# Kernel tuning notes

Measured on AMD Instinct MI355X. Metric: run time of the kernel, lower is better.

The kernel has to match this reference:

```python
import jax, jax.numpy as jnp
import numpy as np

N, C, H, W = 32, 512, 32, 32
S = 2048
INFLUENCE = 1.0  # influence_decay='constant', training_progress irrelevant


def setup_inputs() -> dict:
    key = jax.random.key(0)
    k1, k2 = jax.random.split(key)
    x = jax.random.normal(k1, (N, C, H, W), dtype=jnp.float32)
    # nn.Parameter(torch.randn(S, C) / C)
    codebook = jax.random.normal(k2, (S, C), dtype=jnp.float32) / C
    return {"x": x, "codebook": codebook}


def _distances(x_flat, codebook):
    # x_flat: [N, C, P], codebook: [S, C] -> [N, S, P]
    # same math as ((x[:,None]-cb[None,...,None])**2).sum(2), without the
    # [N, S, C, P] intermediate
    x2 = jnp.sum(x_flat * x_flat, axis=1)          # [N, P]
    c2 = jnp.sum(codebook * codebook, axis=1)      # [S]
    xc = jnp.einsum('ncp,sc->nsp', x_flat, codebook)  # [N, S, P]
    return x2[:, None, :] + c2[None, :, None] - 2.0 * xc


def reference(x, codebook):
    n, c = x.shape[:2]
    x_flat = x.reshape(n, c, -1)                      # [N, C, P]
    xs = jax.lax.stop_gradient(x_flat)                # distance(x_flat.detach())
    d = _distances(xs, codebook)                      # [N, S, P]
    idx = jnp.argmin(d, axis=1)                       # [N, P]
    xq = jnp.transpose(codebook[idx], (0, 2, 1)).reshape(x.shape)  # [N,C,H,W]
    loss_commitment = jnp.mean((x - jax.lax.stop_gradient(xq)) ** 2)
    d_sorted = jnp.sort(d, axis=1)                    # ascending over S
    w = jnp.exp(-jnp.arange(d.shape[1], dtype=jnp.float32) / INFLUENCE)
    loss_codebook = jnp.mean(w[None, :, None] * d_sorted)
    codebook_indices = idx.reshape(n, *x.shape[2:])   # [N, H, W]
    output = x + jax.lax.stop_gradient(xq - x)        # straight-through
    return (loss_codebook, loss_commitment, codebook_indices, output)
```

## Files before the change

kernel.cpp:

```cpp
#include <hip/hip_runtime.h>
#include <hip/hip_fp16.h>

#define N_ 32
#define C_ 512
#define P_ 1024
#define S_ 2048
#define NR_ (N_ * P_)
#define GUARD 6e-3f
#define TSIG 2.3f

typedef __attribute__((ext_vector_type(8))) short sh8;
typedef __attribute__((ext_vector_type(4))) float fx4;

#define WS_XT       0ull
#define WS_XTF      33554432ull
#define WS_CBT      100663296ull
#define WS_C2F      102760448ull
#define WS_X2       102768640ull
#define WS_CNT      102899712ull
#define WS_CANDV    103030784ull
#define WS_CANDS    111419392ull
#define WS_ROWPART  119808000ull
#define WS_COMMIT   120070144ull
#define WS_TOTAL    120201216ull

#define TBLK 2048
#define CVTBLK 512

__device__ __forceinline__ unsigned short f2bf(float f) {
  union { float f; unsigned u; } x; x.f = f;
  unsigned r = x.u + 0x7fffu + ((x.u >> 16) & 1u);
  return (unsigned short)(r >> 16);
}

template <typename T>
__device__ __forceinline__ void load16_lds(const T* g, T* l) {
  __builtin_amdgcn_global_load_lds((const __attribute__((address_space(1))) void*)g,
                                   (__attribute__((address_space(3))) void*)l, 16, 0, 0);
}

__global__ __launch_bounds__(256) void k_prep(const float* __restrict__ x,
                                              const float* __restrict__ cb,
                                              unsigned short* __restrict__ xT,
                                              float* __restrict__ xTf,
                                              unsigned short* __restrict__ cbT,
                                              float* __restrict__ c2f,
                                              float* __restrict__ x2ws,
                                              int* __restrict__ cnt) {
  __shared__ float tile[16][516];
  const int tid = threadIdx.x;
  const int bx = blockIdx.x;

  if (bx < TBLK) {
    const int n = bx >> 6;
    const int p0 = (bx & 63) << 4;
    const float* xb = x + (size_t)n * (C_ * P_) + p0;
    const int pl = tid & 15, ch = tid >> 4;
#pragma unroll 4
    for (int it = 0; it < 32; ++it) {
      int c = it * 16 + ch;
      tile[pl][c] = xb[(size_t)c * P_ + pl];
    }
    __syncthreads();

#pragma unroll
    for (int it = 0; it < 8; ++it) {
      int idx = tid + 256 * it;
      int row = idx >> 7, c4 = (idx & 127) << 2;
      float4 f = *(const float4*)&tile[row][c4];
      size_t R = (size_t)((n << 10) + p0 + row);
      *(float4*)(xTf + R * C_ + c4) = f;
      ushort4 o;
      o.x = f2bf(f.x); o.y = f2bf(f.y); o.z = f2bf(f.z); o.w = f2bf(f.w);
      *(ushort4*)(xT + R * C_ + c4) = o;
    }

    if (tid < 16) {
      float acc = 0.f;
      for (int c = 0; c < C_; ++c) {
        float t = tile[tid][c];
        acc = __fadd_rn(acc, __fmul_rn(t, t));
      }
      int R = (n << 10) + p0 + tid;
      x2ws[R] = acc;
      cnt[R] = 0;
    }
  } else {
    const int s = (bx - TBLK) * 4 + (tid >> 6);
    const int l = tid & 63;
    const float* row = cb + (size_t)s * C_;
    double c2d = 0.0;
#pragma unroll
    for (int h = 0; h < 2; ++h) {
      int c = h * 256 + l * 4;
      float4 v = *(const float4*)(row + c);
      ushort4 o;
      o.x = f2bf(v.x); o.y = f2bf(v.y); o.z = f2bf(v.z); o.w = f2bf(v.w);
      *(ushort4*)(cbT + (size_t)s * C_ + c) = o;
      c2d += (double)__fmul_rn(v.x, v.x) + (double)__fmul_rn(v.y, v.y) +
             (double)__fmul_rn(v.z, v.z) + (double)__fmul_rn(v.w, v.w);
    }
#pragma unroll
    for (int off = 32; off > 0; off >>= 1) c2d += __shfl_down(c2d, off);
    if (l == 0) c2f[s] = (float)c2d;
  }
}

__global__ __launch_bounds__(256, 4) void k_gemm(const unsigned short* __restrict__ xT,
                                                 const unsigned short* __restrict__ cbT,
                                                 const float* __restrict__ x2ws,
                                                 float* __restrict__ candv,
                                                 int* __restrict__ cands,
                                                 int* __restrict__ cnt) {
  __shared__ unsigned short As[128 * 64];
  __shared__ unsigned short Bs[128 * 64];
  __shared__ float t_lds[128];
  const int tid = threadIdx.x;
  const int w = tid >> 6, l = tid & 63;
  const int bx = blockIdx.x;
  const int m_tile = ((bx >> 7) << 3) + (bx & 7);
  const int s_tile = (bx >> 3) & 15;
  const int m0 = m_tile << 7, s0 = s_tile << 7;
  const int wm = (w & 1) << 6, wsf = (w >> 1) << 6;
  const int quad = l >> 4, lane15 = l & 15;

  if (tid < 128) t_lds[tid] = TSIG * __fsqrt_rn(x2ws[m0 + tid]) * (1.0f / 512.0f);

  size_t gA[4], gB[4];
  unsigned short *lA[4], *lB[4];
#pragma unroll
  for (int q = 0; q < 4; ++q) {
    int chunk = (q * 4 + w) * 64 + l;
    int m = chunk >> 3, k8s = chunk & 7;
    int k8 = k8s ^ (m & 7);
    gA[q] = (size_t)(m0 + m) * (C_ * 2) + (size_t)k8 * 16;
    gB[q] = (size_t)(s0 + m) * (C_ * 2) + (size_t)k8 * 16;
    lA[q] = As + (q * 4 + w) * 512;
    lB[q] = Bs + (q * 4 + w) * 512;
  }
  const char* xb = (const char*)xT;
  const char* cbb = (const char*)cbT;

  fx4 acc[4][4];
#pragma unroll
  for (int i = 0; i < 4; ++i)
#pragma unroll
    for (int j = 0; j < 4; ++j) acc[i][j] = (fx4){0.f, 0.f, 0.f, 0.f};

  for (int kk = 0; kk < 8; ++kk) {
#pragma unroll
    for (int q = 0; q < 4; ++q) {
      load16_lds((const unsigned short*)(xb + gA[q] + (size_t)kk * 128), lA[q]);
      load16_lds((const unsigned short*)(cbb + gB[q] + (size_t)kk * 128), lB[q]);
    }
    __syncthreads();
#pragma unroll
    for (int ks = 0; ks < 2; ++ks) {
      const int k8g = ks * 4 + quad;
      sh8 af[4], bf[4];
#pragma unroll
      for (int mi = 0; mi < 4; ++mi) {
        int m = wm + mi * 16 + lane15;
        af[mi] = *(const sh8*)(As + m * 64 + (k8g ^ (m & 7)) * 8);
      }
#pragma unroll
      for (int si = 0; si < 4; ++si) {
        int s = wsf + si * 16 + lane15;
        bf[si] = *(const sh8*)(Bs + s * 64 + (k8g ^ (s & 7)) * 8);
      }
#pragma unroll
      for (int mi = 0; mi < 4; ++mi)
#pragma unroll
        for (int si = 0; si < 4; ++si)
          acc[mi][si] = __builtin_amdgcn_mfma_f32_16x16x32_bf16(af[mi], bf[si], acc[mi][si], 0, 0, 0);
    }
    __syncthreads();
  }

  const unsigned below = (1u << lane15) - 1u;
#pragma unroll
  for (int mi = 0; mi < 4; ++mi) {
#pragma unroll
    for (int r = 0; r < 4; ++r) {
      const int rowl = wm + mi * 16 + quad * 4 + r;
      const int rowg = m0 + rowl;
      const float t = t_lds[rowl];
      float v[4]; int scol[4]; bool hit[4];
      float vmax = -1e30f; int smax = 0;
#pragma unroll
      for (int si = 0; si < 4; ++si) {
        v[si] = acc[mi][si][r];
        scol[si] = s0 + wsf + si * 16 + lane15;
        hit[si] = v[si] >= t;
        if (v[si] > vmax) { vmax = v[si]; smax = scol[si]; }
      }
      int total = 0, myslot[4];
#pragma unroll
      for (int si = 0; si < 4; ++si) {
        unsigned long long b = __ballot(hit[si]);
        unsigned seg = (unsigned)((b >> (quad * 16)) & 0xFFFFull);
        myslot[si] = total + __popc(seg & below);
        total += __popc(seg);
      }
#pragma unroll
      for (int off = 1; off < 16; off <<= 1) {
        float ov = __shfl_xor(vmax, off);
        int os = __shfl_xor(smax, off);
        if (ov > vmax) { vmax = ov; smax = os; }
      }
      int base = 0;
      if (lane15 == 0) base = atomicAdd(&cnt[rowg], total > 0 ? total : 1);
      base = __shfl(base, quad * 16);
      if (total > 0) {
#pragma unroll
        for (int si = 0; si < 4; ++si) {
          if (hit[si]) {
            int slot = base + myslot[si];
            if (slot < 64) {
              candv[(size_t)rowg * 64 + slot] = v[si];
              cands[(size_t)rowg * 64 + slot] = scol[si];
            }
          }
        }
      } else if (lane15 == 0 && base < 64) {
        candv[(size_t)rowg * 64 + base] = vmax;
        cands[(size_t)rowg * 64 + base] = smax;
      }
    }
  }
}

__global__ __launch_bounds__(256, 4) void k_phase2(
    const float* __restrict__ cb, const float* __restrict__ xTf,
    const float* __restrict__ candvG, const int* __restrict__ candsG,
    const int* __restrict__ cntG, const float* __restrict__ c2f,
    const float* __restrict__ x2ws, float* __restrict__ out,
    double* __restrict__ rowpart) {
  __shared__ float xrow[4][C_];
  const int tid = threadIdx.x;
  const int w = tid >> 6, l = tid & 63;
  const int R = blockIdx.x * 4 + w;

  const int cnt = min(cntG[R], 64);
  const float x2f = x2ws[R];
  const bool act = l < cnt;
  float v = candvG[(size_t)R * 64 + l];
  int s = candsG[(size_t)R * 64 + l];
  v = act ? v : -1e30f;
  s = act ? s : 0x7fffffff;
  const int sIdx = act ? s : 0;
  const float dt = act
      ? __fsub_rn(__fadd_rn(x2f, c2f[sIdx]), __fmul_rn(2.f, v))
      : 1e30f;

  float M = v;
#pragma unroll
  for (int off = 1; off < 64; off <<= 1) M = fmaxf(M, __shfl_xor(M, off));

  int rank = 0;
  for (int k = 0; k < 64; ++k) {
    float dk = __shfl(dt, k);
    int sk = __shfl(s, k);
    rank += (dk < dt || (dk == dt && sk < s)) ? 1 : 0;
  }

  double contrib = act ? (double)__expf(-(float)rank) * (double)dt : 0.0;
#pragma unroll
  for (int off = 32; off > 0; off >>= 1) contrib += __shfl_down(contrib, off);
  if (l == 0) rowpart[R] = contrib;

  const bool near = act && (v >= M - GUARD);
  const unsigned long long bal = __ballot(near);
  const int nres = __popcll(bal);
  if (nres == 1) {
    int src = __ffsll(bal) - 1;
    int wins = __shfl(s, src);
    if (l == 0) out[2 + R] = (float)wins;
  } else {
#pragma unroll
    for (int k = 0; k < 2; ++k)
      *(float4*)&xrow[w][l * 8 + k * 4] = *(const float4*)(xTf + (size_t)R * C_ + l * 8 + k * 4);
    float d32 = 1e30f;
    if (near) {
      const float4* crow = (const float4*)(cb + (size_t)s * C_);
      float acc = 0.f;
#pragma unroll 8
      for (int i = 0; i < C_ / 4; ++i) {
        float4 cv = crow[i];
        float4 xv = *(const float4*)&xrow[w][i * 4];
        acc = __fadd_rn(acc, __fmul_rn(xv.x, cv.x));
        acc = __fadd_rn(acc, __fmul_rn(xv.y, cv.y));
        acc = __fadd_rn(acc, __fmul_rn(xv.z, cv.z));
        acc = __fadd_rn(acc, __fmul_rn(xv.w, cv.w));
      }
      d32 = __fsub_rn(__fadd_rn(x2f, c2f[s]), __fmul_rn(2.f, acc));
    }
    float bd = d32;
    int bs2 = near ? s : 0x7fffffff;
#pragma unroll
    for (int off = 1; off < 64; off <<= 1) {
      float ov = __shfl_xor(bd, off);
      int os = __shfl_xor(bs2, off);
      if (ov < bd || (ov == bd && os < bs2)) { bd = ov; bs2 = os; }
    }
    if (l == 0) out[2 + R] = (float)bs2;
  }
}

__global__ __launch_bounds__(256) void k2_output(
    const float* __restrict__ x, const float* __restrict__ cb,
    float* __restrict__ out, double* __restrict__ commit_partial) {
  __shared__ double r2[4];
  const int tid = threadIdx.x;
  const int bx = blockIdx.x;
  const int n = bx >> 9, c = bx & 511;
  const int p = tid * 4;

  const float* xr = x + ((size_t)n * C_ + c) * P_ + p;
  float4 xv = *(const float4*)xr;
  float xs[4] = {xv.x, xv.y, xv.z, xv.w};
  const float* idxf = out + 2 + n * P_ + p;
  float o[4];
  float acc = 0.f;
#pragma unroll
  for (int k = 0; k < 4; ++k) {
    int s = (int)idxf[k];
    float q = cb[(size_t)s * C_ + c];
    float t = __fsub_rn(q, xs[k]);
    o[k] = __fadd_rn(xs[k], t);
    float dd = __fsub_rn(xs[k], q);
    acc += dd * dd;
  }
  float* orow = out + 2 + N_ * P_ + ((size_t)n * C_ + c) * P_ + p;
  ((float2*)orow)[0] = make_float2(o[0], o[1]);
  ((float2*)orow)[1] = make_float2(o[2], o[3]);

  double dacc = (double)acc;
#pragma unroll
  for (int off = 32; off > 0; off >>= 1) dacc += __shfl_down(dacc, off);
  if ((tid & 63) == 0) r2[tid >> 6] = dacc;
  __syncthreads();
  if (tid == 0) commit_partial[bx] = r2[0] + r2[1] + r2[2] + r2[3];
}

__global__ __launch_bounds__(256) void k3_finalize(
    const double* __restrict__ pa, int na, const double* __restrict__ pb, int nb,
    float* __restrict__ out) {
  __shared__ double red[8];
  const int tid = threadIdx.x;
  double a = 0.0, b = 0.0;
  for (int i = tid; i < na; i += 256) a += pa[i];
  for (int i = tid; i < nb; i += 256) b += pb[i];
#pragma unroll
  for (int off = 32; off > 0; off >>= 1) {
    a += __shfl_down(a, off);
    b += __shfl_down(b, off);
  }
  if ((tid & 63) == 0) {
    red[(tid >> 6) * 2 + 0] = a;
    red[(tid >> 6) * 2 + 1] = b;
  }
  __syncthreads();
  if (tid == 0) {
    double A = red[0] + red[2] + red[4] + red[6];
    double B = red[1] + red[3] + red[5] + red[7];
    out[0] = (float)(A / ((double)N_ * (double)S_ * (double)P_));
    out[1] = (float)(B / ((double)N_ * (double)C_ * (double)P_));
  }
}

#define TPW 8
#define KC 32
#define SC 64
#define KCF 48
__global__ __launch_bounds__(256) void k1_fallback(
    const float* __restrict__ x, const float* __restrict__ cb,
    float* __restrict__ out, double* __restrict__ cb_partial) {
  __shared__ float dval[TPW][KCF];
  __shared__ float x2f[TPW];
  __shared__ double redd[4];
  __shared__ float x_t[TPW][C_ + 4];
  __shared__ float cb_t[SC][KC + 4];
  __shared__ int cand_s[TPW][KCF];
  __shared__ _Float16 sc[S_][TPW];

  const int tid = threadIdx.x;
  const int bx = blockIdx.x;
  const int n = bx >> 7;
  const int p0 = (bx & 127) * TPW;

  const float* xn = x + (size_t)n * C_ * P_ + p0;
#pragma unroll
  for (int q = 0; q < 16; ++q) {
    int e = tid + 256 * q;
    int c = e >> 3, j = e & 7;
    x_t[j][c] = xn[(size_t)c * P_ + j];
  }
  __syncthreads();
  if (tid < TPW) {
    float acc = 0.f;
    for (int c = 0; c < C_; ++c)
      acc = __fadd_rn(acc, __fmul_rn(x_t[tid][c], x_t[tid][c]));
    x2f[tid] = acc;
  }
  const int j = tid & 7;
  const int sg = tid >> 3;
  for (int s0 = 0; s0 < S_; s0 += SC) {
    float acc0 = 0.f, acc1 = 0.f;
    for (int k0 = 0; k0 < C_; k0 += KC) {
      __syncthreads();
#pragma unroll
      for (int q = 0; q < 8; ++q) {
        int e = tid + 256 * q;
        int i = e >> 5, cc = e & 31;
        cb_t[i][cc] = cb[(size_t)(s0 + i) * C_ + k0 + cc];
      }
      __syncthreads();
      const float* xr = &x_t[j][k0];
#pragma unroll
      for (int cs = 0; cs < KC; cs += 4) {
        float4 xv = *(const float4*)(xr + cs);
        float4 a4 = *(const float4*)(&cb_t[sg][cs]);
        float4 b4 = *(const float4*)(&cb_t[sg + 32][cs]);
        acc0 += xv.x * a4.x + xv.y * a4.y + xv.z * a4.z + xv.w * a4.w;
        acc1 += xv.x * b4.x + xv.y * b4.y + xv.z * b4.z + xv.w * b4.w;
      }
    }
    sc[s0 + sg][j] = (_Float16)acc0;
    sc[s0 + sg + 32][j] = (_Float16)acc1;
  }
  __syncthreads();
  {
    const int g = tid >> 5, t = tid & 31;
    for (int pass = 0; pass < KCF; ++pass) {
      float bv = -1e30f;
      int bs = 0;
      for (int k = 0; k < 64; ++k) {
        int s = t + 32 * k;
        float vv = (float)sc[s][g];
        if (vv > bv) { bv = vv; bs = s; }
      }
#pragma unroll
      for (int off = 1; off < 32; off <<= 1) {
        float ov = __shfl_xor(bv, off);
        int os = __shfl_xor(bs, off);
        if (ov > bv || (ov == bv && os < bs)) { bv = ov; bs = os; }
      }
      if (t == 0) {
        cand_s[g][pass] = bs;
        sc[bs][g] = (_Float16)(-65504.f);
      }
      __syncthreads();
    }
  }
  for (int task = tid; task < TPW * KCF; task += 256) {
    int jj = task / KCF, r = task % KCF;
    int s = cand_s[jj][r];
    const float* row = cb + (size_t)s * C_;
    const float* xrw = &x_t[jj][0];
    float acc = 0.f;
    double c2d = 0.0;
    for (int c = 0; c < C_; c += 4) {
      float4 cv = *(const float4*)(row + c);
      acc = __fadd_rn(acc, __fmul_rn(xrw[c + 0], cv.x));
      acc = __fadd_rn(acc, __fmul_rn(xrw[c + 1], cv.y));
      acc = __fadd_rn(acc, __fmul_rn(xrw[c + 2], cv.z));
      acc = __fadd_rn(acc, __fmul_rn(xrw[c + 3], cv.w));
      c2d += (double)__fmul_rn(cv.x, cv.x);
      c2d += (double)__fmul_rn(cv.y, cv.y);
      c2d += (double)__fmul_rn(cv.z, cv.z);
      c2d += (double)__fmul_rn(cv.w, cv.w);
    }
    float c2s = (float)c2d;
    dval[jj][r] = __fsub_rn(__fadd_rn(x2f[jj], c2s), __fmul_rn(2.f, acc));
  }
  __syncthreads();
  double contrib = 0.0;
  for (int task = tid; task < TPW * KCF; task += 256) {
    int jj = task / KCF, r = task % KCF;
    float e = dval[jj][r];
    int s = cand_s[jj][r];
    int rank = 0;
    for (int r2 = 0; r2 < KCF; ++r2) {
      float e2 = dval[jj][r2];
      int s2 = cand_s[jj][r2];
      rank += (e2 < e || (e2 == e && s2 < s)) ? 1 : 0;
    }
    contrib += exp((double)(-rank)) * (double)e;
    if (rank == 0) out[2 + n * P_ + p0 + jj] = (float)s;
  }
  __syncthreads();
#pragma unroll
  for (int off = 32; off > 0; off >>= 1) contrib += __shfl_down(contrib, off);
  if ((tid & 63) == 0) redd[tid >> 6] = contrib;
  __syncthreads();
  if (tid == 0) cb_partial[bx] = redd[0] + redd[1] + redd[2] + redd[3];
}

extern "C" void kernel_launch(void* const* d_in, const int* in_sizes, int n_in,
                              void* d_out, int out_size, void* d_ws, size_t ws_size,
                              hipStream_t stream) {
  const float* x = (const float*)d_in[0];
  const float* cb = (const float*)d_in[1];
  float* out = (float*)d_out;
  char* ws = (char*)d_ws;

  if (ws_size >= WS_TOTAL) {
    unsigned short* xT = (unsigned short*)(ws + WS_XT);
    float* xTf = (float*)(ws + WS_XTF);
    unsigned short* cbT = (unsigned short*)(ws + WS_CBT);
    float* c2f = (float*)(ws + WS_C2F);
    float* x2ws = (float*)(ws + WS_X2);
    int* cnt = (int*)(ws + WS_CNT);
    float* candv = (float*)(ws + WS_CANDV);
    int* cands = (int*)(ws + WS_CANDS);
    double* rowpart = (double*)(ws + WS_ROWPART);
    double* commitp = (double*)(ws + WS_COMMIT);

    hipLaunchKernelGGL(k_prep, dim3(TBLK + CVTBLK), dim3(256), 0, stream,
                       x, cb, xT, xTf, cbT, c2f, x2ws, cnt);
    hipLaunchKernelGGL(k_gemm, dim3(4096), dim3(256), 0, stream,
                       xT, cbT, x2ws, candv, cands, cnt);
    hipLaunchKernelGGL(k_phase2, dim3(NR_ / 4), dim3(256), 0, stream,
                       cb, xTf, candv, cands, cnt, c2f, x2ws, out, rowpart);
    hipLaunchKernelGGL(k2_output, dim3(16384), dim3(256), 0, stream, x, cb, out, commitp);
    hipLaunchKernelGGL(k3_finalize, dim3(1), dim3(256), 0, stream,
                       rowpart, NR_, commitp, 16384, out);
  } else {
    double* cb_partial = (double*)d_ws;
    double* commitp = cb_partial + 4096;
    hipLaunchKernelGGL(k1_fallback, dim3(4096), dim3(256), 0, stream, x, cb, out, cb_partial);
    hipLaunchKernelGGL(k2_output, dim3(16384), dim3(256), 0, stream, x, cb, out, commitp);
    hipLaunchKernelGGL(k3_finalize, dim3(1), dim3(256), 0, stream,
                       cb_partial, 4096, commitp, 16384, out);
  }
}
```

Measured before the change: 477.9 us.

## Enlarge GEMM tiles to 256x256 with double-buffered LDS pipeline and vectorized prep loads

Measured after the change: 498.3 us. 1.04x slower.

```diff
diff --git a/kernel.cpp b/kernel.cpp
--- a/kernel.cpp
+++ b/kernel.cpp
@@ -55,11 +55,15 @@
     const int n = bx >> 6;
     const int p0 = (bx & 63) << 4;
     const float* xb = x + (size_t)n * (C_ * P_) + p0;
-    const int pl = tid & 15, ch = tid >> 4;
-#pragma unroll 4
-    for (int it = 0; it < 32; ++it) {
-      int c = it * 16 + ch;
-      tile[pl][c] = xb[(size_t)c * P_ + pl];
+    const int p4 = (tid & 3) << 2, ch = tid >> 2;
+#pragma unroll
+    for (int it = 0; it < 8; ++it) {
+      int c = (it << 6) + ch;
+      float4 v = *(const float4*)(xb + (size_t)c * P_ + p4);
+      tile[p4 + 0][c] = v.x;
+      tile[p4 + 1][c] = v.y;
+      tile[p4 + 2][c] = v.z;
+      tile[p4 + 3][c] = v.w;
     }
     __syncthreads();
 
@@ -106,92 +110,135 @@
   }
 }
 
-__global__ __launch_bounds__(256, 4) void k_gemm(const unsigned short* __restrict__ xT,
+#define KTILE 16384
+
+__global__ __launch_bounds__(512, 2) void k_gemm(const unsigned short* __restrict__ xT,
                                                  const unsigned short* __restrict__ cbT,
                                                  const float* __restrict__ x2ws,
                                                  float* __restrict__ candv,
                                                  int* __restrict__ cands,
                                                  int* __restrict__ cnt) {
-  __shared__ unsigned short As[128 * 64];
-  __shared__ unsigned short Bs[128 * 64];
-  __shared__ float t_lds[128];
+  extern __shared__ unsigned short dynLds[];
+  unsigned short* As = dynLds;
+  unsigned short* Bs = dynLds + 2 * KTILE;
+  __shared__ float t_lds[256];
+
   const int tid = threadIdx.x;
   const int w = tid >> 6, l = tid & 63;
   const int bx = blockIdx.x;
-  const int m_tile = ((bx >> 7) << 3) + (bx & 7);
-  const int s_tile = (bx >> 3) & 15;
-  const int m0 = m_tile << 7, s0 = s_tile << 7;
-  const int wm = (w & 1) << 6, wsf = (w >> 1) << 6;
+  const int xcd = bx & 7, idxx = bx >> 3;
+  const int m_tile = xcd * 16 + (idxx >> 3);
+  const int s_tile = idxx & 7;
+  const int m0 = m_tile << 8, s0 = s_tile << 8;
+  const int wm128 = (w >> 2) << 7;
+  const int wn64 = (w & 3) << 6;
   const int quad = l >> 4, lane15 = l & 15;
 
-  if (tid < 128) t_lds[tid] = TSIG * __fsqrt_rn(x2ws[m0 + tid]) * (1.0f / 512.0f);
-
-  size_t gA[4], gB[4];
-  unsigned short *lA[4], *lB[4];
-#pragma unroll
-  for (int q = 0; q < 4; ++q) {
-    int chunk = (q * 4 + w) * 64 + l;
-    int m = chunk >> 3, k8s = chunk & 7;
-    int k8 = k8s ^ (m & 7);
-    gA[q] = (size_t)(m0 + m) * (C_ * 2) + (size_t)k8 * 16;
-    gB[q] = (size_t)(s0 + m) * (C_ * 2) + (size_t)k8 * 16;
-    lA[q] = As + (q * 4 + w) * 512;
-    lB[q] = Bs + (q * 4 + w) * 512;
-  }
+  if (tid < 256) t_lds[tid] = TSIG * __fsqrt_rn(x2ws[m0 + tid]) * (1.0f / 512.0f);
+
   const char* xb = (const char*)xT;
   const char* cbb = (const char*)cbT;
 
-  fx4 acc[4][4];
-#pragma unroll
-  for (int i = 0; i < 4; ++i)
+  size_t gAoff[4], gBoff[4];
+  unsigned short *lA[4], *lB[4];
+#pragma unroll
+  for (int q = 0; q < 4; ++q) {
+    int c = q * 512 + tid;
+    int m = c >> 3;
+    int k8 = (c & 7) ^ (m & 7);
+    gAoff[q] = (size_t)(m0 + m) * 1024 + (size_t)k8 * 16;
+    gBoff[q] = (size_t)(s0 + m) * 1024 + (size_t)k8 * 16;
+    lA[q] = As + (size_t)c * 8;
+    lB[q] = Bs + (size_t)c * 8;
+  }
+
+  fx4 acc[8][4];
+#pragma unroll
+  for (int i = 0; i < 8; ++i)
 #pragma unroll
     for (int j = 0; j < 4; ++j) acc[i][j] = (fx4){0.f, 0.f, 0.f, 0.f};
 
-  for (int kk = 0; kk < 8; ++kk) {
+  auto STAGE = [&](int kt, int bsel) {
 #pragma unroll
     for (int q = 0; q < 4; ++q) {
-      load16_lds((const unsigned short*)(xb + gA[q] + (size_t)kk * 128), lA[q]);
-      load16_lds((const unsigned short*)(cbb + gB[q] + (size_t)kk * 128), lB[q]);
-    }
-    __syncthreads();
-#pragma unroll
-    for (int ks = 0; ks < 2; ++ks) {
-      const int k8g = ks * 4 + quad;
-      sh8 af[4], bf[4];
-#pragma unroll
-      for (int mi = 0; mi < 4; ++mi) {
-        int m = wm + mi * 16 + lane15;
-        af[mi] = *(const sh8*)(As + m * 64 + (k8g ^ (m & 7)) * 8);
-      }
-#pragma unroll
-      for (int si = 0; si < 4; ++si) {
-        int s = wsf + si * 16 + lane15;
-        bf[si] = *(const sh8*)(Bs + s * 64 + (k8g ^ (s & 7)) * 8);
-      }
+      load16_lds((const unsigned short*)(xb + gAoff[q] + (size_t)kt * 128), lA[q] + bsel * KTILE);
+      load16_lds((const unsigned short*)(cbb + gBoff[q] + (size_t)kt * 128), lB[q] + bsel * KTILE);
+    }
+  };
+
+  STAGE(0, 0);
+  STAGE(1, 1);
+  asm volatile("s_waitcnt vmcnt(8)" ::: "memory");
+  __builtin_amdgcn_s_barrier();
+  asm volatile("" ::: "memory");
+
+  for (int kt = 0; kt < 8; ++kt) {
+    const unsigned short* Ab = As + (kt & 1) * KTILE;
+    const unsigned short* Bb = Bs + (kt & 1) * KTILE;
+    sh8 af[4][2];
+#pragma unroll
+    for (int ph = 0; ph < 4; ++ph) {
+      const int mh = ph >> 1, sh = ph & 1;
+      if (sh == 0) {
+#pragma unroll
+        for (int mi = 0; mi < 4; ++mi) {
+          const int m = wm128 + mh * 64 + mi * 16 + lane15;
+          const int swz = m & 7;
+#pragma unroll
+          for (int ks = 0; ks < 2; ++ks)
+            af[mi][ks] = *(const sh8*)(Ab + m * 64 + (((ks * 4 + quad) ^ swz) << 3));
+        }
+      }
+      sh8 bf[2][2];
+#pragma unroll
+      for (int si = 0; si < 2; ++si) {
+        const int s = wn64 + sh * 32 + si * 16 + lane15;
+        const int swz = s & 7;
+#pragma unroll
+        for (int ks = 0; ks < 2; ++ks)
+          bf[si][ks] = *(const sh8*)(Bb + s * 64 + (((ks * 4 + quad) ^ swz) << 3));
+      }
+      __builtin_amdgcn_s_barrier();
+      __builtin_amdgcn_s_setprio(1);
 #pragma unroll
       for (int mi = 0; mi < 4; ++mi)
 #pragma unroll
-        for (int si = 0; si < 4; ++si)
-          acc[mi][si] = __builtin_amdgcn_mfma_f32_16x16x32_bf16(af[mi], bf[si], acc[mi][si], 0, 0, 0);
-    }
-    __syncthreads();
+        for (int si = 0; si < 2; ++si)
+#pragma unroll
+          for (int ks = 0; ks < 2; ++ks)
+            acc[mh * 4 + mi][sh * 2 + si] = __builtin_amdgcn_mfma_f32_16x16x32_bf16(
+                af[mi][ks], bf[si][ks], acc[mh * 4 + mi][sh * 2 + si], 0, 0, 0);
+      __builtin_amdgcn_s_setprio(0);
+      __builtin_amdgcn_s_barrier();
+      asm volatile("" ::: "memory");
+    }
+    if (kt < 6) {
+      STAGE(kt + 2, kt & 1);
+      asm volatile("s_waitcnt vmcnt(8)" ::: "memory");
+      __builtin_amdgcn_s_barrier();
+      asm volatile("" ::: "memory");
+    } else if (kt == 6) {
+      asm volatile("s_waitcnt vmcnt(0)" ::: "memory");
+      __builtin_amdgcn_s_barrier();
+      asm volatile("" ::: "memory");
+    }
   }
 
   const unsigned below = (1u << lane15) - 1u;
 #pragma unroll
-  for (int mi = 0; mi < 4; ++mi) {
+  for (int mi = 0; mi < 8; ++mi) {
 #pragma unroll
     for (int r = 0; r < 4; ++r) {
-      const int rowl = wm + mi * 16 + quad * 4 + r;
+      const int rowl = wm128 + ((mi >> 2) << 6) + ((mi & 3) << 4) + (quad << 2) + r;
       const int rowg = m0 + rowl;
-      const float t = t_lds[rowl];
+      const float thr = t_lds[rowl];
       float v[4]; int scol[4]; bool hit[4];
       float vmax = -1e30f; int smax = 0;
 #pragma unroll
       for (int si = 0; si < 4; ++si) {
         v[si] = acc[mi][si][r];
-        scol[si] = s0 + wsf + si * 16 + lane15;
-        hit[si] = v[si] >= t;
+        scol[si] = s0 + wn64 + ((si >> 1) << 5) + ((si & 1) << 4) + lane15;
+        hit[si] = v[si] >= thr;
         if (v[si] > vmax) { vmax = v[si]; smax = scol[si]; }
       }
       int total = 0, myslot[4];
@@ -517,9 +564,16 @@
     double* rowpart = (double*)(ws + WS_ROWPART);
     double* commitp = (double*)(ws + WS_COMMIT);
 
+    static bool attr_set = false;
+    if (!attr_set) {
+      (void)hipFuncSetAttribute(reinterpret_cast<const void*>(k_gemm),
+                                hipFuncAttributeMaxDynamicSharedMemorySize, 131072);
+      attr_set = true;
+    }
+
     hipLaunchKernelGGL(k_prep, dim3(TBLK + CVTBLK), dim3(256), 0, stream,
                        x, cb, xT, xTf, cbT, c2f, x2ws, cnt);
-    hipLaunchKernelGGL(k_gemm, dim3(4096), dim3(256), 0, stream,
+    hipLaunchKernelGGL(k_gemm, dim3(1024), dim3(512), 131072, stream,
                        xT, cbT, x2ws, candv, cands, cnt);
     hipLaunchKernelGGL(k_phase2, dim3(NR_ / 4), dim3(256), 0, stream,
                        cb, xTf, candv, cands, cnt, c2f, x2ws, out, rowpart);
```
